# Kernel optimization log

Hardware: AMD Instinct MI355X
Metric: run time of the kernel (lower is better)

The kernel has to match this reference:

```python
import jax, jax.numpy as jnp
import numpy as np


def _warp(input1, input2):
    """Bilinear flow warp. input1: [B,C,H,W] features, input2: [B,2,H,W] flow (dx,dy).
    Out-of-bounds samples contribute zero (matches typical warp_cuda kernels)."""
    B, C, H, W = input1.shape
    # sample coordinates: x = j + flow_x, y = i + flow_y
    gy, gx = jnp.meshgrid(jnp.arange(H, dtype=input1.dtype),
                          jnp.arange(W, dtype=input1.dtype), indexing='ij')
    x = gx[None] + input2[:, 0]  # [B,H,W]
    y = gy[None] + input2[:, 1]

    x0 = jnp.floor(x)
    y0 = jnp.floor(y)
    x1 = x0 + 1.0
    y1 = y0 + 1.0
    # bilinear weights
    wx1 = x - x0
    wx0 = 1.0 - wx1
    wy1 = y - y0
    wy0 = 1.0 - wy1

    img = jnp.transpose(input1, (0, 2, 3, 1))  # [B,H,W,C], channels-last for gather
    bidx = jnp.arange(B)[:, None, None]        # [B,1,1]

    def sample(yy, xx):
        # zero outside bounds
        valid = (yy >= 0) & (yy <= H - 1) & (xx >= 0) & (xx <= W - 1)
        yi = jnp.clip(yy, 0, H - 1).astype(jnp.int32)
        xi = jnp.clip(xx, 0, W - 1).astype(jnp.int32)
        v = img[bidx, yi, xi]  # [B,H,W,C]
        return v * valid[..., None].astype(img.dtype)

    out = (sample(y0, x0) * (wy0 * wx0)[..., None]
           + sample(y0, x1) * (wy0 * wx1)[..., None]
           + sample(y1, x0) * (wy1 * wx0)[..., None]
           + sample(y1, x1) * (wy1 * wx1)[..., None])  # [B,H,W,C]
    return jnp.transpose(out, (0, 3, 1, 2))  # [B,C,H,W]


def setup_inputs() -> dict:
    key = jax.random.key(0)
    k1, k2 = jax.random.split(key)
    B, C, H, W = 8, 64, 256, 448
    input1 = jax.random.normal(k1, (B, C, H, W), dtype=jnp.float32)
    # flow of a few pixels magnitude
    input2 = jax.random.normal(k2, (B, 2, H, W), dtype=jnp.float32) * 4.0
    return {"input1": input1, "input2": input2}


def reference(input1, input2):
    return _warp(input1, input2)
```

## Files before the change

### kernel.cpp

```cpp
#include <hip/hip_runtime.h>

constexpr int B = 8, C = 64, H = 256, W = 448;
constexpr int HW = H * W;
constexpr int NPIX = B * HW;
constexpr int BLK = 256;
constexpr int XCDS = 8;

constexpr int NBLOCKS_V1 = NPIX / BLK;
constexpr int BLOCKS_PER_XCD_V1 = NBLOCKS_V1 / XCDS;

constexpr int TILE = 64;
constexpr int TILES_PER_ROW = W / TILE;
constexpr int TILES_PER_IMG = HW / TILE;
constexpr int NBLOCKS_V2 = B * TILES_PER_IMG;
constexpr int BLOCKS_PER_XCD_V2 = NBLOCKS_V2 / XCDS;
constexpr size_t WS_NEEDED = (size_t)B * HW * C * sizeof(float);

__global__ __launch_bounds__(256) void transpose_kernel(
    const float* __restrict__ img,
    float* __restrict__ tmp)
{
    __shared__ float lds[64][65];

    int blk = blockIdx.x;
    int b   = blk / TILES_PER_IMG;
    int t   = blk - b * TILES_PER_IMG;
    int hw0 = t * TILE;

    int tx = threadIdx.x & 63;
    int ty = threadIdx.x >> 6;

    const float* src = img + (size_t)b * C * HW + hw0 + tx;
    #pragma unroll
    for (int k = 0; k < 16; ++k) {
        int c = ty + 4 * k;
        lds[c][tx] = src[(size_t)c * HW];
    }
    __syncthreads();

    float* dst = tmp + ((size_t)b * HW + hw0) * C + tx;
    #pragma unroll
    for (int k = 0; k < 16; ++k) {
        int px = ty + 4 * k;
        dst[(size_t)px * C] = lds[tx][px];
    }
}

__global__ __launch_bounds__(256) void gather_kernel(
    const float* __restrict__ tmp,
    const float* __restrict__ flow,
    float* __restrict__ out)
{
    __shared__ float sm[64][65];

    int bid = blockIdx.x;
    int swz = (bid % XCDS) * BLOCKS_PER_XCD_V2 + (bid / XCDS);

    int b  = swz / TILES_PER_IMG;
    int t  = swz - b * TILES_PER_IMG;
    int i  = t / TILES_PER_ROW;
    int j0 = (t - i * TILES_PER_ROW) * TILE;

    int lane = threadIdx.x & 63;
    int wv   = threadIdx.x >> 6;

    const float* fb = flow + (size_t)b * 2 * HW;
    const size_t img_base = (size_t)b * H * (size_t)W;

    #pragma unroll 4
    for (int pp = 0; pp < 16; ++pp) {
        int p  = wv * 16 + pp;
        int j  = j0 + p;
        int ij = i * W + j;

        float fx = fb[ij];
        float fy = fb[HW + ij];

        float x = (float)j + fx;
        float y = (float)i + fy;

        float x0f = floorf(x), y0f = floorf(y);
        int   x0  = (int)x0f,  y0  = (int)y0f;
        float wx1 = x - x0f,   wy1 = y - y0f;
        float wx0 = 1.0f - wx1, wy0 = 1.0f - wy1;

        bool vx0 = (x0 >= 0)  & (x0 <= W - 1);
        bool vx1 = (x0 >= -1) & (x0 <= W - 2);
        bool vy0 = (y0 >= 0)  & (y0 <= H - 1);
        bool vy1 = (y0 >= -1) & (y0 <= H - 2);

        float w00 = (vy0 & vx0) ? wy0 * wx0 : 0.0f;
        float w01 = (vy0 & vx1) ? wy0 * wx1 : 0.0f;
        float w10 = (vy1 & vx0) ? wy1 * wx0 : 0.0f;
        float w11 = (vy1 & vx1) ? wy1 * wx1 : 0.0f;

        int xi0 = min(max(x0, 0),     W - 1);
        int xi1 = min(max(x0 + 1, 0), W - 1);
        int yi0 = min(max(y0, 0),     H - 1);
        int yi1 = min(max(y0 + 1, 0), H - 1);

        const float* r0 = tmp + (img_base + (size_t)yi0 * W) * C + lane;
        const float* r1 = tmp + (img_base + (size_t)yi1 * W) * C + lane;
        float v00 = r0[(size_t)xi0 * C];
        float v01 = r0[(size_t)xi1 * C];
        float v10 = r1[(size_t)xi0 * C];
        float v11 = r1[(size_t)xi1 * C];

        sm[p][lane] = w00 * v00 + w01 * v01 + w10 * v10 + w11 * v11;
    }
    __syncthreads();

    int px = threadIdx.x & 63;
    int cg = threadIdx.x >> 6;
    float* ob = out + (size_t)b * C * HW + (size_t)i * W + j0 + px;
    #pragma unroll
    for (int k = 0; k < 16; ++k) {
        int c = cg + 4 * k;
        ob[(size_t)c * HW] = sm[px][c];
    }
}

__global__ __launch_bounds__(256) void warp_kernel(
    const float* __restrict__ img,
    const float* __restrict__ flow,
    float* __restrict__ out)
{
    int bid = blockIdx.x;
    int swz = (bid % XCDS) * BLOCKS_PER_XCD_V1 + (bid / XCDS);
    int pix = swz * BLK + threadIdx.x;

    int b  = pix / HW;
    int ij = pix - b * HW;
    int i  = ij / W;
    int j  = ij - i * W;

    float fx = flow[(size_t)(b * 2 + 0) * HW + ij];
    float fy = flow[(size_t)(b * 2 + 1) * HW + ij];

    float x = (float)j + fx;
    float y = (float)i + fy;

    float x0f = floorf(x), y0f = floorf(y);
    int   x0  = (int)x0f,  y0  = (int)y0f;
    float wx1 = x - x0f,   wy1 = y - y0f;
    float wx0 = 1.0f - wx1, wy0 = 1.0f - wy1;

    bool vx0 = (x0 >= 0)  & (x0 <= W - 1);
    bool vx1 = (x0 >= -1) & (x0 <= W - 2);
    bool vy0 = (y0 >= 0)  & (y0 <= H - 1);
    bool vy1 = (y0 >= -1) & (y0 <= H - 2);

    float w00 = (vy0 & vx0) ? wy0 * wx0 : 0.0f;
    float w01 = (vy0 & vx1) ? wy0 * wx1 : 0.0f;
    float w10 = (vy1 & vx0) ? wy1 * wx0 : 0.0f;
    float w11 = (vy1 & vx1) ? wy1 * wx1 : 0.0f;

    int xi0 = min(max(x0, 0),     W - 1);
    int xi1 = min(max(x0 + 1, 0), W - 1);
    int yi0 = min(max(y0, 0),     H - 1);
    int yi1 = min(max(y0 + 1, 0), H - 1);

    int o00 = yi0 * W + xi0;
    int o01 = yi0 * W + xi1;
    int o10 = yi1 * W + xi0;
    int o11 = yi1 * W + xi1;

    const float* ib = img + (size_t)b * C * HW;
    float*       ob = out + (size_t)b * C * HW + ij;

    #pragma unroll
    for (int cb = 0; cb < C; cb += 8) {
        float v00[8], v01[8], v10[8], v11[8];
        #pragma unroll
        for (int u = 0; u < 8; ++u) {
            const float* q = ib + (size_t)(cb + u) * HW;
            v00[u] = q[o00];
            v01[u] = q[o01];
            v10[u] = q[o10];
            v11[u] = q[o11];
        }
        #pragma unroll
        for (int u = 0; u < 8; ++u) {
            ob[(size_t)(cb + u) * HW] =
                w00 * v00[u] + w01 * v01[u] + w10 * v10[u] + w11 * v11[u];
        }
    }
}

extern "C" void kernel_launch(void* const* d_in, const int* in_sizes, int n_in,
                              void* d_out, int out_size, void* d_ws, size_t ws_size,
                              hipStream_t stream) {
    const float* img  = (const float*)d_in[0];
    const float* flow = (const float*)d_in[1];
    float* out = (float*)d_out;

    if (ws_size >= WS_NEEDED && d_ws != nullptr) {
        float* tmp = (float*)d_ws;
        transpose_kernel<<<dim3(NBLOCKS_V2), dim3(BLK), 0, stream>>>(img, tmp);
        gather_kernel<<<dim3(NBLOCKS_V2), dim3(BLK), 0, stream>>>(tmp, flow, out);
    } else {
        warp_kernel<<<dim3(NBLOCKS_V1), dim3(BLK), 0, stream>>>(img, flow, out);
    }
}
```

Before: 528.3 us.

## Vectorize transpose and output stores, compute per-pixel coords once per lane with readlane broadcast

The transpose kernel now loads and stores float4 instead of scalars, with the LDS tile indexing adjusted to match. In the gather kernel, each of 16 lanes computes one pixel's bilinear offsets and weights once. These are broadcast to the whole wave with readlane instead of being recomputed redundantly by all 64 lanes, and byte offsets use 32-bit arithmetic. The output write-back now uses float4 stores from a channel-major LDS tile. The aim is fewer memory instructions and less redundant ALU work, at the cost of possible LDS bank conflicts in the strided reads.

Result: faster. 509.9 us (-3.5%).

```diff
diff --git a/kernel.cpp b/kernel.cpp
--- a/kernel.cpp
+++ b/kernel.cpp
@@ -27,22 +27,32 @@
     int t   = blk - b * TILES_PER_IMG;
     int hw0 = t * TILE;
 
-    int tx = threadIdx.x & 63;
-    int ty = threadIdx.x >> 6;
-
-    const float* src = img + (size_t)b * C * HW + hw0 + tx;
-    #pragma unroll
-    for (int k = 0; k < 16; ++k) {
-        int c = ty + 4 * k;
-        lds[c][tx] = src[(size_t)c * HW];
+    int pc = threadIdx.x & 15;
+    int cg = threadIdx.x >> 4;
+    const float* src = img + (size_t)b * C * HW + hw0 + 4 * pc;
+    #pragma unroll
+    for (int k = 0; k < 4; ++k) {
+        int c = cg + 16 * k;
+        float4 v = *(const float4*)(src + (size_t)c * HW);
+        lds[c][4 * pc + 0] = v.x;
+        lds[c][4 * pc + 1] = v.y;
+        lds[c][4 * pc + 2] = v.z;
+        lds[c][4 * pc + 3] = v.w;
     }
     __syncthreads();
 
-    float* dst = tmp + ((size_t)b * HW + hw0) * C + tx;
-    #pragma unroll
-    for (int k = 0; k < 16; ++k) {
-        int px = ty + 4 * k;
-        dst[(size_t)px * C] = lds[tx][px];
+    int lc = threadIdx.x & 15;
+    int pg = threadIdx.x >> 4;
+    float* dst = tmp + ((size_t)b * HW + hw0) * C + 4 * lc;
+    #pragma unroll
+    for (int k = 0; k < 4; ++k) {
+        int px = pg + 16 * k;
+        float4 v;
+        v.x = lds[4 * lc + 0][px];
+        v.y = lds[4 * lc + 1][px];
+        v.z = lds[4 * lc + 2][px];
+        v.w = lds[4 * lc + 3][px];
+        *(float4*)(dst + (size_t)px * C) = v;
     }
 }
 
@@ -64,59 +74,83 @@
     int lane = threadIdx.x & 63;
     int wv   = threadIdx.x >> 6;
 
+    int pl = lane & 15;
+    int p1 = wv * 16 + pl;
+    int j  = j0 + p1;
+    int ij = i * W + j;
+
     const float* fb = flow + (size_t)b * 2 * HW;
-    const size_t img_base = (size_t)b * H * (size_t)W;
+    float fx = fb[ij];
+    float fy = fb[HW + ij];
+
+    float x = (float)j + fx;
+    float y = (float)i + fy;
+
+    float x0f = floorf(x), y0f = floorf(y);
+    int   x0  = (int)x0f,  y0  = (int)y0f;
+    float wx1 = x - x0f,   wy1 = y - y0f;
+    float wx0 = 1.0f - wx1, wy0 = 1.0f - wy1;
+
+    bool vx0 = (x0 >= 0)  & (x0 <= W - 1);
+    bool vx1 = (x0 >= -1) & (x0 <= W - 2);
+    bool vy0 = (y0 >= 0)  & (y0 <= H - 1);
+    bool vy1 = (y0 >= -1) & (y0 <= H - 2);
+
+    float w00r = (vy0 & vx0) ? wy0 * wx0 : 0.0f;
+    float w01r = (vy0 & vx1) ? wy0 * wx1 : 0.0f;
+    float w10r = (vy1 & vx0) ? wy1 * wx0 : 0.0f;
+    float w11r = (vy1 & vx1) ? wy1 * wx1 : 0.0f;
+
+    int xi0 = min(max(x0, 0),     W - 1);
+    int xi1 = min(max(x0 + 1, 0), W - 1);
+    int yi0 = min(max(y0, 0),     H - 1);
+    int yi1 = min(max(y0 + 1, 0), H - 1);
+
+    int o00r = (yi0 * W + xi0) << 8;
+    int o01r = (yi0 * W + xi1) << 8;
+    int o10r = (yi1 * W + xi0) << 8;
+    int o11r = (yi1 * W + xi1) << 8;
+
+    const char* tb = (const char*)(tmp + (size_t)b * HW * C);
 
     #pragma unroll 4
     for (int pp = 0; pp < 16; ++pp) {
-        int p  = wv * 16 + pp;
-        int j  = j0 + p;
-        int ij = i * W + j;
-
-        float fx = fb[ij];
-        float fy = fb[HW + ij];
-
-        float x = (float)j + fx;
-        float y = (float)i + fy;
-
-        float x0f = floorf(x), y0f = floorf(y);
-        int   x0  = (int)x0f,  y0  = (int)y0f;
-        float wx1 = x - x0f,   wy1 = y - y0f;
-        float wx0 = 1.0f - wx1, wy0 = 1.0f - wy1;
-
-        bool vx0 = (x0 >= 0)  & (x0 <= W - 1);
-        bool vx1 = (x0 >= -1) & (x0 <= W - 2);
-        bool vy0 = (y0 >= 0)  & (y0 <= H - 1);
-        bool vy1 = (y0 >= -1) & (y0 <= H - 2);
-
-        float w00 = (vy0 & vx0) ? wy0 * wx0 : 0.0f;
-        float w01 = (vy0 & vx1) ? wy0 * wx1 : 0.0f;
-        float w10 = (vy1 & vx0) ? wy1 * wx0 : 0.0f;
-        float w11 = (vy1 & vx1) ? wy1 * wx1 : 0.0f;
-
-        int xi0 = min(max(x0, 0),     W - 1);
-        int xi1 = min(max(x0 + 1, 0), W - 1);
-        int yi0 = min(max(y0, 0),     H - 1);
-        int yi1 = min(max(y0 + 1, 0), H - 1);
-
-        const float* r0 = tmp + (img_base + (size_t)yi0 * W) * C + lane;
-        const float* r1 = tmp + (img_base + (size_t)yi1 * W) * C + lane;
-        float v00 = r0[(size_t)xi0 * C];
-        float v01 = r0[(size_t)xi1 * C];
-        float v10 = r1[(size_t)xi0 * C];
-        float v11 = r1[(size_t)xi1 * C];
-
-        sm[p][lane] = w00 * v00 + w01 * v01 + w10 * v10 + w11 * v11;
+        int   o00 = __builtin_amdgcn_readlane(o00r, pp);
+        int   o01 = __builtin_amdgcn_readlane(o01r, pp);
+        int   o10 = __builtin_amdgcn_readlane(o10r, pp);
+        int   o11 = __builtin_amdgcn_readlane(o11r, pp);
+        float w00 = __int_as_float(__builtin_amdgcn_readlane(__float_as_int(w00r), pp));
+        float w01 = __int_as_float(__builtin_amdgcn_readlane(__float_as_int(w01r), pp));
+        float w10 = __int_as_float(__builtin_amdgcn_readlane(__float_as_int(w10r), pp));
+        float w11 = __int_as_float(__builtin_amdgcn_readlane(__float_as_int(w11r), pp));
+
+        const float* q00 = (const float*)(tb + (unsigned)o00);
+        const float* q01 = (const float*)(tb + (unsigned)o01);
+        const float* q10 = (const float*)(tb + (unsigned)o10);
+        const float* q11 = (const float*)(tb + (unsigned)o11);
+
+        float v00 = q00[lane];
+        float v01 = q01[lane];
+        float v10 = q10[lane];
+        float v11 = q11[lane];
+
+        float acc = w00 * v00 + w01 * v01 + w10 * v10 + w11 * v11;
+        sm[lane][wv * 16 + pp] = acc;
     }
     __syncthreads();
 
-    int px = threadIdx.x & 63;
-    int cg = threadIdx.x >> 6;
-    float* ob = out + (size_t)b * C * HW + (size_t)i * W + j0 + px;
-    #pragma unroll
-    for (int k = 0; k < 16; ++k) {
-        int c = cg + 4 * k;
-        ob[(size_t)c * HW] = sm[px][c];
+    int pg = threadIdx.x & 15;
+    int cg = threadIdx.x >> 4;
+    float* ob = out + (size_t)b * C * HW + (size_t)i * W + j0 + 4 * pg;
+    #pragma unroll
+    for (int k = 0; k < 4; ++k) {
+        int c = cg + 16 * k;
+        float4 v;
+        v.x = sm[c][4 * pg + 0];
+        v.y = sm[c][4 * pg + 1];
+        v.z = sm[c][4 * pg + 2];
+        v.w = sm[c][4 * pg + 3];
+        *(float4*)(ob + (size_t)c * HW) = v;
     }
 }
 
```
